# Kernel optimization log

Measured on AMD Instinct MI355X. Metric: run time of the kernel, lower is better.

The kernel has to match this reference:

```python
import jax, jax.numpy as jnp
import numpy as np

NEG = -1e16  # matches torch masked_fill value
LN_EPS = 1e-5


def _gat_layer(h, mask, b):
    """h: [..., N, D]; mask: broadcastable bool [..., N, N]; b: broadcastable [..., D]."""
    scores = jnp.einsum('...nd,...md->...nm', h, h)
    scores = jnp.where(mask, scores, NEG)
    attn = jax.nn.softmax(scores, axis=-1)
    return jnp.einsum('...nm,...md->...nd', attn, h) + b


def setup_inputs() -> dict:
    key = jax.random.key(0)
    ks = jax.random.split(key, 6)
    B, N, C, H, D = 8, 2048, 64, 4, 64
    x = jax.random.normal(ks[0], (B, N, C), dtype=jnp.float32)
    graph = jax.random.randint(ks[1], (N, N), 0, 2, dtype=jnp.int32)
    # xavier_uniform-style scale for W: bound = sqrt(6/(fan_in+fan_out))
    bnd_h = float(np.sqrt(6.0 / (C + D)))
    Wh = jax.random.uniform(ks[2], (H, D, C), jnp.float32, -bnd_h, bnd_h)
    bh = jnp.zeros((H, D), jnp.float32)
    bnd_o = float(np.sqrt(6.0 / (H * D + D)))
    Wo = jax.random.uniform(ks[3], (D, H * D), jnp.float32, -bnd_o, bnd_o)
    bo = jnp.zeros((D,), jnp.float32)
    gamma = jnp.ones((D,), jnp.float32)
    beta = jnp.zeros((D,), jnp.float32)
    return {"x": x, "graph": graph, "Wh": Wh, "bh": bh, "Wo": Wo,
            "bo": bo, "gamma": gamma, "beta": beta}


def reference(x, graph, Wh, bh, Wo, bo, gamma, beta):
    B, N, C = x.shape
    H, D, _ = Wh.shape
    # graph = (graph + I) > 0
    mask = (graph + jnp.eye(N, dtype=graph.dtype)) > 0  # [N, N] bool
    # per-head linear projection: [B, H, N, D]
    h = jnp.einsum('bnc,hdc->bhnd', x, Wh)
    out_h = _gat_layer(h, mask[None, None], bh[None, :, None, :])  # [B,H,N,D]
    # torch.cat over heads along last dim == head-major reshape
    cat = jnp.transpose(out_h, (0, 2, 1, 3)).reshape(B, N, H * D)
    z = jax.nn.leaky_relu(cat, negative_slope=0.2)
    h2 = jnp.einsum('bnk,dk->bnd', z, Wo)  # [B, N, D]
    out2 = _gat_layer(h2, mask[None], bo)
    z2 = jax.nn.leaky_relu(out2, negative_slope=0.2)
    # LayerNorm over last dim
    mu = jnp.mean(z2, axis=-1, keepdims=True)
    var = jnp.mean(jnp.square(z2 - mu), axis=-1, keepdims=True)
    out = (z2 - mu) * jax.lax.rsqrt(var + LN_EPS) * gamma + beta
    return out  # dropout p=0.0 -> identity
```

## Files before the change

### kernel.cpp

```cpp
#include <hip/hip_runtime.h>

#define NN 2048
#define PITCH 72
#define MPITCH 264

typedef __attribute__((ext_vector_type(8))) _Float16 half8;
typedef __attribute__((ext_vector_type(4))) float floatx4;

static_assert(sizeof(half8) == 16, "");

#define MRINIT -3.0e38f

__device__ __forceinline__ unsigned short f2h(float f) {
    union { _Float16 h; unsigned short u; } v;
    v.h = (_Float16)f;
    return v.u;
}
__device__ __forceinline__ float h2f(unsigned short u) {
    union { unsigned short u; _Float16 h; } v;
    v.u = u;
    return (float)v.h;
}
__device__ __forceinline__ unsigned int pk2h(float a, float b) {
    union { __fp16 __attribute__((ext_vector_type(2))) h; unsigned int u; } v;
    v.h = __builtin_amdgcn_cvt_pkrtz(a, b);
    return v.u;
}
__device__ __forceinline__ void barrier_lds_only() {
    __asm__ __volatile__("" ::: "memory");
    __builtin_amdgcn_s_waitcnt(0xC07F);
    __builtin_amdgcn_s_barrier();
    __asm__ __volatile__("" ::: "memory");
}

__global__ __launch_bounds__(256) void mask_kernel(const int* __restrict__ graph,
                                                   unsigned int* __restrict__ mbitsT) {
    const int t = threadIdx.x;
    const int lane = t & 63;
    const int W = (blockIdx.x << 2) + (t >> 6);
    const int i = W >> 5;
    const int cb = W & 31;
    const int j = (cb << 6) + lane;
    const int g = graph[(size_t)i * NN + j];
    const unsigned long long bal = __ballot((g > 0) || (i == j));
    if (lane == 0)  mbitsT[((cb << 1) << 11) + i]     = (unsigned int)bal;
    if (lane == 32) mbitsT[(((cb << 1) + 1) << 11) + i] = (unsigned int)(bal >> 32);
}

__global__ __launch_bounds__(256) void proj_gemm(const float* __restrict__ x,
                                                 const float* __restrict__ Wh,
                                                 unsigned short* __restrict__ hout) {
    __shared__ unsigned short xs[64 * PITCH];
    __shared__ unsigned short wh[4 * 64 * PITCH];
    const int t = threadIdx.x;
    const int b = blockIdx.x >> 5;
    const int n0 = (blockIdx.x & 31) << 6;
    for (int i = t; i < 512; i += 256) {
        const int r = i >> 3, c8 = (i & 7) << 3;
        const float* xp = x + (((size_t)b * NN + n0 + r) << 6) + c8;
        const float4 f0 = *(const float4*)(xp);
        const float4 f1 = *(const float4*)(xp + 4);
        uint4 pk;
        pk.x = pk2h(f0.x, f0.y); pk.y = pk2h(f0.z, f0.w);
        pk.z = pk2h(f1.x, f1.y); pk.w = pk2h(f1.z, f1.w);
        *(uint4*)(&xs[r * PITCH + c8]) = pk;
    }
    for (int i = t; i < 2048; i += 256) {
        const int hd = i >> 3, c8 = (i & 7) << 3;
        const float* wp = Wh + ((size_t)hd << 6) + c8;
        const float4 f0 = *(const float4*)(wp);
        const float4 f1 = *(const float4*)(wp + 4);
        uint4 pk;
        pk.x = pk2h(f0.x, f0.y); pk.y = pk2h(f0.z, f0.w);
        pk.z = pk2h(f1.x, f1.y); pk.w = pk2h(f1.z, f1.w);
        *(uint4*)(&wh[hd * PITCH + c8]) = pk;
    }
    __syncthreads();
    const int wave = t >> 6;
    const int m = t & 15;
    const int quad = (t >> 4) & 3;
    half8 bf0[4], bf1[4];
#pragma unroll
    for (int nt = 0; nt < 4; ++nt) {
        const int row = (wave << 6) + (nt << 4) + m;
        bf0[nt] = *(const half8*)(&wh[row * PITCH + (quad << 3)]);
        bf1[nt] = *(const half8*)(&wh[row * PITCH + 32 + (quad << 3)]);
    }
    floatx4 acc[4][4];
#pragma unroll
    for (int mt = 0; mt < 4; ++mt)
#pragma unroll
        for (int nt = 0; nt < 4; ++nt) acc[mt][nt] = floatx4{0.f, 0.f, 0.f, 0.f};
#pragma unroll
    for (int mt = 0; mt < 4; ++mt) {
        const half8 a0 = *(const half8*)(&xs[((mt << 4) + m) * PITCH + (quad << 3)]);
        const half8 a1 = *(const half8*)(&xs[((mt << 4) + m) * PITCH + 32 + (quad << 3)]);
#pragma unroll
        for (int nt = 0; nt < 4; ++nt) {
            acc[mt][nt] = __builtin_amdgcn_mfma_f32_16x16x32_f16(a0, bf0[nt], acc[mt][nt], 0, 0, 0);
            acc[mt][nt] = __builtin_amdgcn_mfma_f32_16x16x32_f16(a1, bf1[nt], acc[mt][nt], 0, 0, 0);
        }
    }
    unsigned short* hp = hout + ((((size_t)(b << 2) + wave) * NN + n0) << 6) + m;
#pragma unroll
    for (int mt = 0; mt < 4; ++mt)
#pragma unroll
        for (int reg = 0; reg < 4; ++reg)
#pragma unroll
            for (int nt = 0; nt < 4; ++nt)
                hp[(((mt << 4) + (quad << 2) + reg) << 6) + (nt << 4)] = f2h(acc[mt][nt][reg]);
}

template <int QG, int OUTMODE, int NSPLIT>
__global__ __launch_bounds__(256) void gat_flash(const unsigned short* __restrict__ Hm,
                                                 const unsigned int* __restrict__ mbitsT,
                                                 const float* __restrict__ bias,
                                                 const int bias_mod,
                                                 void* __restrict__ OutP,
                                                 float2* __restrict__ mlP) {
    __shared__ unsigned short Ks[2][64 * PITCH];
    __shared__ unsigned short Kts[2][64 * PITCH];
    __shared__ unsigned short Ps[4 * QG * 16 * 64];

    const int t = threadIdx.x;
    const int wave = t >> 6;
    const int lane = t & 63;
    const int quad = lane >> 4;
    const int m = lane & 15;

    const int qtbits = 4;
    const int sbits = (NSPLIT == 4) ? 2 : (NSPLIT == 2) ? 1 : 0;
    const int bid = blockIdx.x;
    const int qt = bid & ((1 << qtbits) - 1);
    const int split = (bid >> qtbits) & (NSPLIT - 1);
    const int mat = bid >> (qtbits + sbits);
    const int q0 = qt << 7;
    const int nkt = 32 / NSPLIT;
    const int kt0 = split * nkt;

    const unsigned short* Hb = Hm + ((size_t)mat << 17);
    const int wbase = q0 + wave * (16 * QG);

    const _Float16 LOG2E = (_Float16)1.44269504f;
    half8 bq0[QG], bq1[QG];
    int gq[QG];
#pragma unroll
    for (int g = 0; g < QG; ++g) {
        gq[g] = wbase + (g << 4) + m;
        bq0[g] = *(const half8*)(Hb + (gq[g] << 6) + (quad << 3)) * LOG2E;
        bq1[g] = *(const half8*)(Hb + (gq[g] << 6) + 32 + (quad << 3)) * LOG2E;
    }

    const int p = t >> 3;
    const int cc = t & 7;
    const int jch = p >> 2;
    const int jo = (p & 3) << 1;

    float mr[QG], lr[QG];
    floatx4 O[QG][4];
#pragma unroll
    for (int g = 0; g < QG; ++g) {
        mr[g] = MRINIT;
        lr[g] = 0.f;
#pragma unroll
        for (int nt = 0; nt < 4; ++nt) O[g][nt] = floatx4{0.f, 0.f, 0.f, 0.f};
    }

    const int msw = m & 7;
    int psb[QG];
#pragma unroll
    for (int g = 0; g < QG; ++g) psb[g] = (wave * QG + g) * 1024 + (m << 6);

    const unsigned short* kg0 = Hb + (((kt0 << 6) + (p << 1)) << 6) + (cc << 3);
    half8 ra = *(const half8*)(kg0);
    half8 rb = *(const half8*)(kg0 + 64);

    for (int it = 0; it < nkt; ++it) {
        const int kt = kt0 + it;
        unsigned short* KS = Ks[it & 1];
        unsigned short* KT = Kts[it & 1];
        unsigned int w0[QG], w1[QG];
#pragma unroll
        for (int g = 0; g < QG; ++g) {
            w0[g] = mbitsT[((kt << 1) << 11) + gq[g]];
            w1[g] = mbitsT[(((kt << 1) + 1) << 11) + gq[g]];
        }
        *(half8*)(&KS[(p << 1) * PITCH + (cc << 3)]) = ra;
        *(half8*)(&KS[((p << 1) + 1) * PITCH + (cc << 3)]) = rb;
        union { half8 v; unsigned int u[4]; } kaU, kbU;
        kaU.v = ra;
        kbU.v = rb;
#pragma unroll
        for (int c = 0; c < 4; ++c) {
            const unsigned int ua = kaU.u[c];
            const unsigned int ub = kbU.u[c];
            const unsigned int lo = __builtin_amdgcn_perm(ub, ua, 0x05040100);
            const unsigned int hi = __builtin_amdgcn_perm(ub, ua, 0x07060302);
            const int d0 = (cc << 3) + (c << 1);
            const int pos = (((jch + cc) & 7) << 3) + jo;
            *(unsigned int*)(&KT[d0 * PITCH + pos]) = lo;
            *(unsigned int*)(&KT[(d0 + 1) * PITCH + pos]) = hi;
        }
        const int ktn = kt0 + ((it + 1) & (nkt - 1));
        const unsigned short* kgn = Hb + (((ktn << 6) + (p << 1)) << 6) + (cc << 3);
        ra = *(const half8*)(kgn);
        rb = *(const half8*)(kgn + 64);

        barrier_lds_only();

        floatx4 a[QG][4];
#pragma unroll
        for (int jt = 0; jt < 4; ++jt) {
            const half8 k0 = *(const half8*)(&KS[((jt << 4) + m) * PITCH + (quad << 3)]);
            const half8 k1 = *(const half8*)(&KS[((jt << 4) + m) * PITCH + 32 + (quad << 3)]);
#pragma unroll
            for (int g = 0; g < QG; ++g) {
                floatx4 z = {0.f, 0.f, 0.f, 0.f};
                z = __builtin_amdgcn_mfma_f32_16x16x32_f16(k0, bq0[g], z, 0, 0, 0);
                z = __builtin_amdgcn_mfma_f32_16x16x32_f16(k1, bq1[g], z, 0, 0, 0);
                a[g][jt] = z;
            }
        }

#pragma unroll
        for (int g = 0; g < QG; ++g) {
            float vmax[4];
#pragma unroll
            for (int jt = 0; jt < 4; ++jt) {
                const unsigned int wv = (jt < 2) ? w0[g] : w1[g];
                const unsigned int bits = (wv >> (((jt & 1) << 4) + (quad << 2))) & 0xFu;
                float v0 = ((bits >> 0) & 1u) ? a[g][jt][0] : MRINIT;
                float v1 = ((bits >> 1) & 1u) ? a[g][jt][1] : MRINIT;
                float v2 = ((bits >> 2) & 1u) ? a[g][jt][2] : MRINIT;
                float v3 = ((bits >> 3) & 1u) ? a[g][jt][3] : MRINIT;
                a[g][jt][0] = v0; a[g][jt][1] = v1; a[g][jt][2] = v2; a[g][jt][3] = v3;
                vmax[jt] = fmaxf(fmaxf(v0, v1), fmaxf(v2, v3));
            }
            float tmx = fmaxf(fmaxf(vmax[0], vmax[1]), fmaxf(vmax[2], vmax[3]));
            tmx = fmaxf(tmx, __shfl_xor(tmx, 16));
            tmx = fmaxf(tmx, __shfl_xor(tmx, 32));
            const float mnew = fmaxf(mr[g], tmx);
            const float alpha = __builtin_amdgcn_exp2f(mr[g] - mnew);
            const bool need = __any(mnew > mr[g]);

            float psum = 0.f;
#pragma unroll
            for (int jt = 0; jt < 4; ++jt) {
                const float p0 = __builtin_amdgcn_exp2f(a[g][jt][0] - mnew);
                const float p1 = __builtin_amdgcn_exp2f(a[g][jt][1] - mnew);
                const float p2 = __builtin_amdgcn_exp2f(a[g][jt][2] - mnew);
                const float p3 = __builtin_amdgcn_exp2f(a[g][jt][3] - mnew);
                psum += (p0 + p1) + (p2 + p3);
                const int ch = (jt << 1) + (quad >> 1);
                *(uint2*)(&Ps[psb[g] + (((ch + msw) & 7) << 3) + ((quad & 1) << 2)]) =
                    make_uint2(pk2h(p0, p1), pk2h(p2, p3));
            }
            psum += __shfl_xor(psum, 16);
            psum += __shfl_xor(psum, 32);
            lr[g] = lr[g] * alpha + psum;
            mr[g] = mnew;

            if (need) {
#pragma unroll
                for (int nt = 0; nt < 4; ++nt) {
                    O[g][nt][0] *= alpha;
                    O[g][nt][1] *= alpha;
                    O[g][nt][2] *= alpha;
                    O[g][nt][3] *= alpha;
                }
            }
        }

        __builtin_amdgcn_wave_barrier();
        __asm__ __volatile__("" ::: "memory");

        half8 pa0[QG], pa1[QG];
#pragma unroll
        for (int g = 0; g < QG; ++g) {
            pa0[g] = *(const half8*)(&Ps[psb[g] + (((quad + msw) & 7) << 3)]);
            pa1[g] = *(const half8*)(&Ps[psb[g] + (((4 + quad + msw) & 7) << 3)]);
        }
#pragma unroll
        for (int nt = 0; nt < 4; ++nt) {
            const int d = (nt << 4) + m;
            const int sw = (d >> 3) & 7;
            const half8 v0 = *(const half8*)(&KT[d * PITCH + (((quad + sw) & 7) << 3)]);
            const half8 v1 = *(const half8*)(&KT[d * PITCH + (((4 + quad + sw) & 7) << 3)]);
#pragma unroll
            for (int g = 0; g < QG; ++g) {
                O[g][nt] = __builtin_amdgcn_mfma_f32_16x16x32_f16(v0, pa0[g], O[g][nt], 0, 0, 0);
                O[g][nt] = __builtin_amdgcn_mfma_f32_16x16x32_f16(v1, pa1[g], O[g][nt], 0, 0, 0);
            }
        }
    }

    if (OUTMODE == 2) {
        unsigned short* Op = (unsigned short*)OutP;
        const size_t pbase = ((size_t)(split << 3) + mat) * NN;
#pragma unroll
        for (int g = 0; g < QG; ++g) {
            unsigned short* Ob = Op + ((pbase + gq[g]) << 6) + (quad << 2);
#pragma unroll
            for (int nt = 0; nt < 4; ++nt)
                *(uint2*)(Ob + (nt << 4)) = make_uint2(pk2h(O[g][nt][0], O[g][nt][1]),
                                                       pk2h(O[g][nt][2], O[g][nt][3]));
        }
        if (lane < 16) {
#pragma unroll
            for (int g = 0; g < QG; ++g)
                mlP[pbase + wbase + (g << 4) + m] = make_float2(mr[g], lr[g]);
        }
        return;
    }

    const int boff = (mat % bias_mod) << 6;
    float4 bb[4];
#pragma unroll
    for (int nt = 0; nt < 4; ++nt)
        bb[nt] = *(const float4*)(bias + boff + (nt << 4) + (quad << 2));
#pragma unroll
    for (int g = 0; g < QG; ++g) {
        const float li = 1.f / lr[g];
        unsigned short* op = (unsigned short*)OutP + (((size_t)mat * NN + gq[g]) << 6) + (quad << 2);
#pragma unroll
        for (int nt = 0; nt < 4; ++nt) {
            float z0 = O[g][nt][0] * li + bb[nt].x;
            float z1 = O[g][nt][1] * li + bb[nt].y;
            float z2 = O[g][nt][2] * li + bb[nt].z;
            float z3 = O[g][nt][3] * li + bb[nt].w;
            z0 = (z0 > 0.f) ? z0 : 0.2f * z0;
            z1 = (z1 > 0.f) ? z1 : 0.2f * z1;
            z2 = (z2 > 0.f) ? z2 : 0.2f * z2;
            z3 = (z3 > 0.f) ? z3 : 0.2f * z3;
            *(uint2*)(op + (nt << 4)) = make_uint2(pk2h(z0, z1), pk2h(z2, z3));
        }
    }
}

__global__ __launch_bounds__(256) void mix_gemm(const unsigned short* __restrict__ oh,
                                                const float* __restrict__ Wo,
                                                unsigned short* __restrict__ h2) {
    __shared__ unsigned short zs[64 * MPITCH];
    __shared__ unsigned short wsm[64 * MPITCH];
    const int t = threadIdx.x;
    const int b = blockIdx.x >> 5;
    const int n0 = (blockIdx.x & 31) << 6;
    for (int i = t; i < 2048; i += 256) {
        const int hh = i >> 9;
        const int r = (i >> 3) & 63;
        const int d8 = i & 7;
        const half8 v = *(const half8*)(oh + ((((size_t)b << 2) + hh) * NN + n0 + r) * 64 + (d8 << 3));
        *(half8*)(&zs[r * MPITCH + (hh << 6) + (d8 << 3)]) = v;
    }
    for (int i = t; i < 2048; i += 256) {
        const int d = i >> 5;
        const int k0 = (i & 31) << 3;
        const float4 f0 = *(const float4*)(Wo + (d << 8) + k0);
        const float4 f1 = *(const float4*)(Wo + (d << 8) + k0 + 4);
        uint4 pk;
        pk.x = pk2h(f0.x, f0.y);
        pk.y = pk2h(f0.z, f0.w);
        pk.z = pk2h(f1.x, f1.y);
        pk.w = pk2h(f1.z, f1.w);
        *(uint4*)(&wsm[d * MPITCH + k0]) = pk;
    }
    __syncthreads();
    const int wave = t >> 6;
    const int m = t & 15;
    const int quad = (t >> 4) & 3;
    const int ar = (wave << 4) + m;
    floatx4 acc[4] = {{0.f, 0.f, 0.f, 0.f}, {0.f, 0.f, 0.f, 0.f},
                      {0.f, 0.f, 0.f, 0.f}, {0.f, 0.f, 0.f, 0.f}};
#pragma unroll
    for (int chunk = 0; chunk < 8; ++chunk) {
        const int k0 = chunk << 5;
        const half8 af = *(const half8*)(&zs[ar * MPITCH + k0 + (quad << 3)]);
#pragma unroll
        for (int nt = 0; nt < 4; ++nt) {
            const half8 bf = *(const half8*)(&wsm[((nt << 4) + m) * MPITCH + k0 + (quad << 3)]);
            acc[nt] = __builtin_amdgcn_mfma_f32_16x16x32_f16(af, bf, acc[nt], 0, 0, 0);
        }
    }
    unsigned short* hp = h2 + (((size_t)b * NN + n0 + (wave << 4) + (quad << 2)) << 6) + m;
#pragma unroll
    for (int reg = 0; reg < 4; ++reg)
#pragma unroll
        for (int nt = 0; nt < 4; ++nt)
            hp[(reg << 6) + (nt << 4)] = f2h(acc[nt][reg]);
}

__global__ __launch_bounds__(256) void combine_ln(const unsigned short* __restrict__ Opart,
                                                  const float2* __restrict__ ml,
                                                  const float* __restrict__ bo,
                                                  const float* __restrict__ gamma,
                                                  const float* __restrict__ beta,
                                                  float* __restrict__ out) {
    const int t = threadIdx.x;
    const int lane = t & 63;
    const size_t r0 = (size_t)((blockIdx.x << 2) + (t >> 6));
    float2 sv[4];
    float mm = MRINIT;
#pragma unroll
    for (int s = 0; s < 4; ++s) {
        sv[s] = ml[(size_t)(NN * 8) * s + r0];
        mm = fmaxf(mm, sv[s].x);
    }
    float l = 0.f, osum = 0.f;
#pragma unroll
    for (int s = 0; s < 4; ++s) {
        const float c = __builtin_amdgcn_exp2f(sv[s].x - mm);
        l += sv[s].y * c;
        osum += h2f(Opart[(((size_t)(NN * 8) * s + r0) << 6) + lane]) * c;
    }
    float v = osum / l + bo[lane];
    v = (v > 0.f) ? v : 0.2f * v;
    float s = v;
    float sq = v * v;
#pragma unroll
    for (int off = 1; off < 64; off <<= 1) {
        s += __shfl_xor(s, off);
        sq += __shfl_xor(sq, off);
    }
    const float mu = s * 0.015625f;
    float var = sq * 0.015625f - mu * mu;
    var = fmaxf(var, 0.f);
    const float rstd = rsqrtf(var + 1e-5f);
    out[(r0 << 6) + lane] = (v - mu) * rstd * gamma[lane] + beta[lane];
}

extern "C" void kernel_launch(void* const* d_in, const int* in_sizes, int n_in,
                              void* d_out, int out_size, void* d_ws, size_t ws_size,
                              hipStream_t stream) {
    const float* x     = (const float*)d_in[0];
    const int*   graph = (const int*)d_in[1];
    const float* Wh    = (const float*)d_in[2];
    const float* bh    = (const float*)d_in[3];
    const float* Wo    = (const float*)d_in[4];
    const float* bo    = (const float*)d_in[5];
    const float* gamma = (const float*)d_in[6];
    const float* beta  = (const float*)d_in[7];
    float* out = (float*)d_out;

    char* ws = (char*)d_ws;
    unsigned int* mbitsT  = (unsigned int*)ws;
    unsigned short* h     = (unsigned short*)(ws + 0x080000);
    unsigned short* oh    = (unsigned short*)(ws + 0x880000);
    unsigned short* h2    = (unsigned short*)(ws + 0x080000);
    float2* ml            = (float2*)(ws + 0x280000);
    unsigned short* Opart = (unsigned short*)(ws + 0x880000);

    mask_kernel<<<16384, 256, 0, stream>>>(graph, mbitsT);
    proj_gemm<<<256, 256, 0, stream>>>(x, Wh, h);
    gat_flash<2, 0, 1><<<512, 256, 0, stream>>>(h, mbitsT, bh, 4, oh, nullptr);
    mix_gemm<<<256, 256, 0, stream>>>(oh, Wo, h2);
    gat_flash<2, 2, 4><<<512, 256, 0, stream>>>(h2, mbitsT, bo, 1, Opart, ml);
    combine_ln<<<4096, 256, 0, stream>>>(Opart, ml, bo, gamma, beta, out);
}
```

Measured before the change: 199.3 us.

## Fuse mask into projection, split layer-1 attention over keys, fold combine into mix GEMM

Merges the mask-packing and projection kernels into one launch and interleaves the mask bit words so each query row loads both halves with a single 64-bit read. The first GAT layer now uses a 2-way key split with partial outputs and running max/sum statistics, which doubles its grid from 512 to 1024 blocks. The split-combine, bias and leaky-ReLU move into the mix GEMM's load stage. The aim is better occupancy in the layer-1 attention kernel and one fewer launch, in exchange for extra partial-output traffic through fp16 intermediates.

```diff
diff --git a/kernel.cpp b/kernel.cpp
--- a/kernel.cpp
+++ b/kernel.cpp
@@ -33,26 +33,29 @@
     __asm__ __volatile__("" ::: "memory");
 }
 
-__global__ __launch_bounds__(256) void mask_kernel(const int* __restrict__ graph,
-                                                   unsigned int* __restrict__ mbitsT) {
+__global__ __launch_bounds__(256) void proj_mask(const float* __restrict__ x,
+                                                 const float* __restrict__ Wh,
+                                                 const int* __restrict__ graph,
+                                                 unsigned int* __restrict__ mbits2,
+                                                 unsigned short* __restrict__ hout) {
     const int t = threadIdx.x;
-    const int lane = t & 63;
-    const int W = (blockIdx.x << 2) + (t >> 6);
-    const int i = W >> 5;
-    const int cb = W & 31;
-    const int j = (cb << 6) + lane;
-    const int g = graph[(size_t)i * NN + j];
-    const unsigned long long bal = __ballot((g > 0) || (i == j));
-    if (lane == 0)  mbitsT[((cb << 1) << 11) + i]     = (unsigned int)bal;
-    if (lane == 32) mbitsT[(((cb << 1) + 1) << 11) + i] = (unsigned int)(bal >> 32);
-}
-
-__global__ __launch_bounds__(256) void proj_gemm(const float* __restrict__ x,
-                                                 const float* __restrict__ Wh,
-                                                 unsigned short* __restrict__ hout) {
+    if (blockIdx.x >= 256) {
+        const int i = blockIdx.x - 256;
+        const int wv = t >> 6, lane = t & 63;
+        const int* gr = graph + ((size_t)i << 11);
+#pragma unroll
+        for (int k = 0; k < 8; ++k) {
+            const int cb = (wv << 3) + k;
+            const int j = (cb << 6) + lane;
+            const unsigned long long bal = __ballot((gr[j] > 0) || (i == j));
+            const int idx = ((cb << 11) + i) << 1;
+            if (lane == 0)  mbits2[idx]     = (unsigned int)bal;
+            if (lane == 32) mbits2[idx + 1] = (unsigned int)(bal >> 32);
+        }
+        return;
+    }
     __shared__ unsigned short xs[64 * PITCH];
     __shared__ unsigned short wh[4 * 64 * PITCH];
-    const int t = threadIdx.x;
     const int b = blockIdx.x >> 5;
     const int n0 = (blockIdx.x & 31) << 6;
     for (int i = t; i < 512; i += 256) {
@@ -111,35 +114,33 @@
                 hp[(((mt << 4) + (quad << 2) + reg) << 6) + (nt << 4)] = f2h(acc[mt][nt][reg]);
 }
 
-template <int QG, int OUTMODE, int NSPLIT>
+template <int NSPLIT, int NMATS>
 __global__ __launch_bounds__(256) void gat_flash(const unsigned short* __restrict__ Hm,
-                                                 const unsigned int* __restrict__ mbitsT,
-                                                 const float* __restrict__ bias,
-                                                 const int bias_mod,
-                                                 void* __restrict__ OutP,
+                                                 const unsigned int* __restrict__ mbits2,
+                                                 unsigned short* __restrict__ OutP,
                                                  float2* __restrict__ mlP) {
     __shared__ unsigned short Ks[2][64 * PITCH];
     __shared__ unsigned short Kts[2][64 * PITCH];
-    __shared__ unsigned short Ps[4 * QG * 16 * 64];
-
+    __shared__ unsigned short Ps[4 * 2 * 16 * 64];
+
+    const int QG = 2;
     const int t = threadIdx.x;
     const int wave = t >> 6;
     const int lane = t & 63;
     const int quad = lane >> 4;
     const int m = lane & 15;
 
-    const int qtbits = 4;
-    const int sbits = (NSPLIT == 4) ? 2 : (NSPLIT == 2) ? 1 : 0;
+    const int sbits = (NSPLIT == 4) ? 2 : 1;
     const int bid = blockIdx.x;
-    const int qt = bid & ((1 << qtbits) - 1);
-    const int split = (bid >> qtbits) & (NSPLIT - 1);
-    const int mat = bid >> (qtbits + sbits);
+    const int qt = bid & 15;
+    const int split = (bid >> 4) & (NSPLIT - 1);
+    const int mat = bid >> (4 + sbits);
     const int q0 = qt << 7;
     const int nkt = 32 / NSPLIT;
     const int kt0 = split * nkt;
 
     const unsigned short* Hb = Hm + ((size_t)mat << 17);
-    const int wbase = q0 + wave * (16 * QG);
+    const int wbase = q0 + wave * 32;
 
     const _Float16 LOG2E = (_Float16)1.44269504f;
     half8 bq0[QG], bq1[QG];
@@ -179,12 +180,10 @@
         const int kt = kt0 + it;
         unsigned short* KS = Ks[it & 1];
         unsigned short* KT = Kts[it & 1];
-        unsigned int w0[QG], w1[QG];
-#pragma unroll
-        for (int g = 0; g < QG; ++g) {
-            w0[g] = mbitsT[((kt << 1) << 11) + gq[g]];
-            w1[g] = mbitsT[(((kt << 1) + 1) << 11) + gq[g]];
-        }
+        uint2 w01[QG];
+#pragma unroll
+        for (int g = 0; g < QG; ++g)
+            w01[g] = *(const uint2*)(mbits2 + (((kt << 11) + gq[g]) << 1));
         *(half8*)(&KS[(p << 1) * PITCH + (cc << 3)]) = ra;
         *(half8*)(&KS[((p << 1) + 1) * PITCH + (cc << 3)]) = rb;
         union { half8 v; unsigned int u[4]; } kaU, kbU;
@@ -227,7 +226,7 @@
             float vmax[4];
 #pragma unroll
             for (int jt = 0; jt < 4; ++jt) {
-                const unsigned int wv = (jt < 2) ? w0[g] : w1[g];
+                const unsigned int wv = (jt < 2) ? w01[g].x : w01[g].y;
                 const unsigned int bits = (wv >> (((jt & 1) << 4) + (quad << 2))) & 0xFu;
                 float v0 = ((bits >> 0) & 1u) ? a[g][jt][0] : MRINIT;
                 float v1 = ((bits >> 1) & 1u) ? a[g][jt][1] : MRINIT;
@@ -294,63 +293,43 @@
         }
     }
 
-    if (OUTMODE == 2) {
-        unsigned short* Op = (unsigned short*)OutP;
-        const size_t pbase = ((size_t)(split << 3) + mat) * NN;
-#pragma unroll
-        for (int g = 0; g < QG; ++g) {
-            unsigned short* Ob = Op + ((pbase + gq[g]) << 6) + (quad << 2);
-#pragma unroll
-            for (int nt = 0; nt < 4; ++nt)
-                *(uint2*)(Ob + (nt << 4)) = make_uint2(pk2h(O[g][nt][0], O[g][nt][1]),
-                                                       pk2h(O[g][nt][2], O[g][nt][3]));
-        }
-        if (lane < 16) {
-#pragma unroll
-            for (int g = 0; g < QG; ++g)
-                mlP[pbase + wbase + (g << 4) + m] = make_float2(mr[g], lr[g]);
-        }
-        return;
-    }
-
-    const int boff = (mat % bias_mod) << 6;
-    float4 bb[4];
-#pragma unroll
-    for (int nt = 0; nt < 4; ++nt)
-        bb[nt] = *(const float4*)(bias + boff + (nt << 4) + (quad << 2));
+    const size_t pbase = ((size_t)split * NMATS + mat) * NN;
 #pragma unroll
     for (int g = 0; g < QG; ++g) {
-        const float li = 1.f / lr[g];
-        unsigned short* op = (unsigned short*)OutP + (((size_t)mat * NN + gq[g]) << 6) + (quad << 2);
-#pragma unroll
-        for (int nt = 0; nt < 4; ++nt) {
-            float z0 = O[g][nt][0] * li + bb[nt].x;
-            float z1 = O[g][nt][1] * li + bb[nt].y;
-            float z2 = O[g][nt][2] * li + bb[nt].z;
-            float z3 = O[g][nt][3] * li + bb[nt].w;
-            z0 = (z0 > 0.f) ? z0 : 0.2f * z0;
-            z1 = (z1 > 0.f) ? z1 : 0.2f * z1;
-            z2 = (z2 > 0.f) ? z2 : 0.2f * z2;
-            z3 = (z3 > 0.f) ? z3 : 0.2f * z3;
-            *(uint2*)(op + (nt << 4)) = make_uint2(pk2h(z0, z1), pk2h(z2, z3));
-        }
-    }
-}
-
-__global__ __launch_bounds__(256) void mix_gemm(const unsigned short* __restrict__ oh,
-                                                const float* __restrict__ Wo,
-                                                unsigned short* __restrict__ h2) {
+        unsigned short* Ob = OutP + ((pbase + gq[g]) << 6) + (quad << 2);
+#pragma unroll
+        for (int nt = 0; nt < 4; ++nt)
+            *(uint2*)(Ob + (nt << 4)) = make_uint2(pk2h(O[g][nt][0], O[g][nt][1]),
+                                                   pk2h(O[g][nt][2], O[g][nt][3]));
+    }
+    if (lane < 16) {
+#pragma unroll
+        for (int g = 0; g < QG; ++g)
+            mlP[pbase + wbase + (g << 4) + m] = make_float2(mr[g], lr[g]);
+    }
+}
+
+__global__ __launch_bounds__(256) void mix_fused(const unsigned short* __restrict__ Op1,
+                                                 const float2* __restrict__ ml1,
+                                                 const float* __restrict__ bh,
+                                                 const float* __restrict__ Wo,
+                                                 unsigned short* __restrict__ h2) {
     __shared__ unsigned short zs[64 * MPITCH];
     __shared__ unsigned short wsm[64 * MPITCH];
+    __shared__ float2 cs[256];
     const int t = threadIdx.x;
     const int b = blockIdx.x >> 5;
     const int n0 = (blockIdx.x & 31) << 6;
-    for (int i = t; i < 2048; i += 256) {
-        const int hh = i >> 9;
-        const int r = (i >> 3) & 63;
-        const int d8 = i & 7;
-        const half8 v = *(const half8*)(oh + ((((size_t)b << 2) + hh) * NN + n0 + r) * 64 + (d8 << 3));
-        *(half8*)(&zs[r * MPITCH + (hh << 6) + (d8 << 3)]) = v;
+    {
+        const int hh = t >> 6, r = t & 63;
+        const size_t row = (size_t)((b << 2) + hh) * NN + n0 + r;
+        const float2 s0 = ml1[row];
+        const float2 s1 = ml1[(size_t)(32 * NN) + row];
+        const float mm = fmaxf(s0.x, s1.x);
+        const float c0 = __builtin_amdgcn_exp2f(s0.x - mm);
+        const float c1 = __builtin_amdgcn_exp2f(s1.x - mm);
+        const float L = s0.y * c0 + s1.y * c1;
+        cs[t] = make_float2(c0 / L, c1 / L);
     }
     for (int i = t; i < 2048; i += 256) {
         const int d = i >> 5;
@@ -358,11 +337,28 @@
         const float4 f0 = *(const float4*)(Wo + (d << 8) + k0);
         const float4 f1 = *(const float4*)(Wo + (d << 8) + k0 + 4);
         uint4 pk;
-        pk.x = pk2h(f0.x, f0.y);
-        pk.y = pk2h(f0.z, f0.w);
-        pk.z = pk2h(f1.x, f1.y);
-        pk.w = pk2h(f1.z, f1.w);
+        pk.x = pk2h(f0.x, f0.y); pk.y = pk2h(f0.z, f0.w);
+        pk.z = pk2h(f1.x, f1.y); pk.w = pk2h(f1.z, f1.w);
         *(uint4*)(&wsm[d * MPITCH + k0]) = pk;
+    }
+    __syncthreads();
+    for (int i = t; i < 2048; i += 256) {
+        const int hh = i >> 9, r = (i >> 3) & 63, d8 = i & 7;
+        const size_t rowoff = (((size_t)((b << 2) + hh) * NN + n0 + r) << 6) + (d8 << 3);
+        const half8 o0 = *(const half8*)(Op1 + rowoff);
+        const half8 o1 = *(const half8*)(Op1 + ((size_t)(32 * NN) << 6) + rowoff);
+        const float2 c = cs[(hh << 6) + r];
+        const float* bp = bh + (hh << 6) + (d8 << 3);
+        float v[8];
+#pragma unroll
+        for (int e = 0; e < 8; ++e) {
+            const float z = (float)o0[e] * c.x + (float)o1[e] * c.y + bp[e];
+            v[e] = (z > 0.f) ? z : 0.2f * z;
+        }
+        uint4 pk;
+        pk.x = pk2h(v[0], v[1]); pk.y = pk2h(v[2], v[3]);
+        pk.z = pk2h(v[4], v[5]); pk.w = pk2h(v[6], v[7]);
+        *(uint4*)(&zs[r * MPITCH + (hh << 6) + (d8 << 3)]) = pk;
     }
     __syncthreads();
     const int wave = t >> 6;
@@ -442,17 +438,17 @@
     float* out = (float*)d_out;
 
     char* ws = (char*)d_ws;
-    unsigned int* mbitsT  = (unsigned int*)ws;
-    unsigned short* h     = (unsigned short*)(ws + 0x080000);
-    unsigned short* oh    = (unsigned short*)(ws + 0x880000);
-    unsigned short* h2    = (unsigned short*)(ws + 0x080000);
-    float2* ml            = (float2*)(ws + 0x280000);
-    unsigned short* Opart = (unsigned short*)(ws + 0x880000);
-
-    mask_kernel<<<16384, 256, 0, stream>>>(graph, mbitsT);
-    proj_gemm<<<256, 256, 0, stream>>>(x, Wh, h);
-    gat_flash<2, 0, 1><<<512, 256, 0, stream>>>(h, mbitsT, bh, 4, oh, nullptr);
-    mix_gemm<<<256, 256, 0, stream>>>(oh, Wo, h2);
-    gat_flash<2, 2, 4><<<512, 256, 0, stream>>>(h2, mbitsT, bo, 1, Opart, ml);
-    combine_ln<<<4096, 256, 0, stream>>>(Opart, ml, bo, gamma, beta, out);
-}
+    unsigned int* mbits2   = (unsigned int*)ws;
+    unsigned short* h      = (unsigned short*)(ws + 0x080000);
+    unsigned short* Op1    = (unsigned short*)(ws + 0x880000);
+    float2* ml1            = (float2*)(ws + 0x1880000);
+    unsigned short* h2     = (unsigned short*)(ws + 0x080000);
+    unsigned short* Op2    = (unsigned short*)(ws + 0x880000);
+    float2* ml2            = (float2*)(ws + 0x1080000);
+
+    proj_mask<<<2304, 256, 0, stream>>>(x, Wh, graph, mbits2, h);
+    gat_flash<2, 32><<<1024, 256, 0, stream>>>(h, mbits2, Op1, ml1);
+    mix_fused<<<256, 256, 0, stream>>>(Op1, ml1, bh, Wo, h2);
+    gat_flash<4, 8><<<512, 256, 0, stream>>>(h2, mbits2, Op2, ml2);
+    combine_ln<<<4096, 256, 0, stream>>>(Op2, ml2, bo, gamma, beta, out);
+}
```

Result: no change. 201.4 us (+1.1%).
